# Performance work log

Hardware: AMD Instinct MI355X
Metric: run time of the kernel (lower is better)

## Reference

```python
import jax, jax.numpy as jnp
import numpy as np

LN_EPS = 1e-5
N_HEADS = 8
N_POINTS = 4


def layer_norm(x, g, b):
    m = x.mean(-1, keepdims=True)
    v = ((x - m) ** 2).mean(-1, keepdims=True)
    return (x - m) / jnp.sqrt(v + LN_EPS) * g + b


def msda(query, ref, src, ts, lsi, mask, Wv, bv, Wo, bo, Wa, ba, Wp, bp):
    # 1D multi-scale deformable attention (temporal, as in PDVC/SAGA-DVC).
    B, Lq, D = query.shape
    Lin = src.shape[0] * 0 + src.shape[1]
    ts_np = np.asarray(ts)
    lsi_np = np.asarray(lsi)
    L = ts_np.shape[0]
    H, P = N_HEADS, N_POINTS
    Dh = D // H
    value = src @ Wv + bv
    value = jnp.where(mask[..., None], 0.0, value).reshape(B, Lin, H, Dh)
    off = (query @ Wo + bo).reshape(B, Lq, H, L, P)
    aw = jax.nn.softmax((query @ Wa + ba).reshape(B, Lq, H, L * P), axis=-1)
    aw = aw.reshape(B, Lq, H, L, P)
    norm = jnp.asarray(ts_np).astype(query.dtype)  # (L,)
    # sampling locations in normalized [0,1] coords: (B,Lq,H,L,P)
    loc = ref[:, :, None, :, None, 0] + off / norm[None, None, None, :, None]
    b_idx = jnp.arange(B)[:, None, None, None]
    h_idx = jnp.arange(H)[None, None, :, None]
    out = jnp.zeros((B, Lq, H, Dh), query.dtype)
    for l in range(L):  # small fixed number of levels
        T = int(ts_np[l]); s = int(lsi_np[l])
        v = value[:, s:s + T]  # (B,T,H,Dh)
        # grid_sample align_corners=False: pixel pos = loc*T - 0.5
        pos = loc[:, :, :, l, :] * T - 0.5  # (B,Lq,H,P)
        x0 = jnp.floor(pos)
        w1 = (pos - x0)[..., None]
        x0i = x0.astype(jnp.int32)

        def gather(xi):
            valid = ((xi >= 0) & (xi < T))[..., None].astype(v.dtype)
            xc = jnp.clip(xi, 0, T - 1)
            return v[b_idx, xc, h_idx] * valid  # (B,Lq,H,P,Dh), zeros pad

        samp = gather(x0i) * (1.0 - w1) + gather(x0i + 1) * w1
        out = out + (samp * aw[:, :, :, l, :, None]).sum(axis=3)
    out = out.reshape(B, Lq, D) @ Wp + bp
    return out, loc, aw


def ffn(x, W1, b1, W2, b2, ln2_g, ln2_b):
    h = jax.nn.relu(x @ W1 + b1) @ W2 + b2
    return layer_norm(x + h, ln2_g, ln2_b)


def setup_inputs() -> dict:
    key = jax.random.key(0)
    ks = jax.random.split(key, 24)
    B, S, D = 8, 3840, 256
    L = 4
    ts = jnp.array([2048, 1024, 512, 256], dtype=jnp.int32)
    lsi = jnp.array([0, 2048, 3072, 3584], dtype=jnp.int32)
    HP = N_HEADS * L * N_POINTS  # 128
    sc = 0.02
    inp = {
        'video_src': jax.random.normal(ks[0], (B, S, D), jnp.float32),
        'audio_src': jax.random.normal(ks[1], (B, S, D), jnp.float32),
        'video_pos': jax.random.normal(ks[2], (B, S, D), jnp.float32),
        'audio_pos': jax.random.normal(ks[3], (B, S, D), jnp.float32),
        'video_ref': jax.random.uniform(ks[4], (B, S, L, 1), jnp.float32),
        'audio_ref': jax.random.uniform(ks[5], (B, S, L, 1), jnp.float32),
        'video_ts': ts, 'video_lsi': lsi,
        'video_mask': jnp.zeros((B, S), jnp.bool_),
        'audio_ts': ts, 'audio_lsi': lsi,
        'audio_mask': jnp.zeros((B, S), jnp.bool_),
        'Wv': jax.random.normal(ks[6], (D, D)) * sc, 'bv': jnp.zeros((D,)),
        'Wo': jax.random.normal(ks[7], (D, HP)) * sc, 'bo': jnp.zeros((HP,)),
        'Wa': jax.random.normal(ks[8], (D, HP)) * sc, 'ba': jnp.zeros((HP,)),
        'Wp': jax.random.normal(ks[9], (D, D)) * sc, 'bp': jnp.zeros((D,)),
        'ln1_g': jnp.ones((D,)), 'ln1_b': jnp.zeros((D,)),
        'W1': jax.random.normal(ks[10], (D, 1024)) * sc, 'b1': jnp.zeros((1024,)),
        'W2': jax.random.normal(ks[11], (1024, D)) * sc, 'b2': jnp.zeros((D,)),
        'ln2_g': jnp.ones((D,)), 'ln2_b': jnp.zeros((D,)),
    }
    return inp


def reference(video_src, audio_src, video_pos, audio_pos, video_ref, audio_ref,
              video_ts, video_lsi, video_mask, audio_ts, audio_lsi, audio_mask,
              Wv, bv, Wo, bo, Wa, ba, Wp, bp, ln1_g, ln1_b,
              W1, b1, W2, b2, ln2_g, ln2_b):
    attn = (Wv, bv, Wo, bo, Wa, ba, Wp, bp)
    # modality self-attention (dropout = identity at eval)
    v2, _, _ = msda(video_src + video_pos, video_ref, video_src,
                    video_ts, video_lsi, video_mask, *attn)
    video = layer_norm(video_src + v2, ln1_g, ln1_b)
    a2, _, _ = msda(audio_src + audio_pos, audio_ref, audio_src,
                    audio_ts, audio_lsi, audio_mask, *attn)
    audio = layer_norm(audio_src + a2, ln1_g, ln1_b)
    # cross-modal deformable attention
    vaa, a_loc, a_aw = msda(audio, audio_ref, video,
                            video_ts, video_lsi, video_mask, *attn)
    aav, v_loc, v_aw = msda(video, video_ref, audio,
                            audio_ts, audio_lsi, audio_mask, *attn)
    vaa = ffn(vaa, W1, b1, W2, b2, ln2_g, ln2_b)
    aav = ffn(aav, W1, b1, W2, b2, ln2_g, ln2_b)
    return (aav, vaa, v_loc, v_aw, a_loc, a_aw)
```

## Files before the change

### kernel.cpp

```cpp
#include <hip/hip_runtime.h>
#include <hip/hip_bf16.h>
#include <cstdint>

#define BB 8
#define SS 3840
#define RR (BB*SS)
#define NHALF ((size_t)RR * 256)

typedef short s16x8 __attribute__((ext_vector_type(8)));
typedef float f32x4 __attribute__((ext_vector_type(4)));

__device__ __forceinline__ ushort f2bf(float f) {
    uint32_t u = __builtin_bit_cast(uint32_t, f);
    u += 0x7FFFu + ((u >> 16) & 1u);
    return (ushort)(u >> 16);
}
__device__ __forceinline__ float bf2f(ushort h) {
    return __builtin_bit_cast(float, (uint32_t)h << 16);
}

#define GLDS16(gp, lp) __builtin_amdgcn_global_load_lds( \
    (const __attribute__((address_space(1))) uint32_t*)(gp), \
    (__attribute__((address_space(3))) uint32_t*)(lp), 16, 0, 0)

__global__ __launch_bounds__(256) void wtrans_all(
    const float* __restrict__ Wv, const float* __restrict__ Wo,
    const float* __restrict__ Wa, const float* __restrict__ Wp,
    const float* __restrict__ W1, const float* __restrict__ W2,
    const float* __restrict__ bo, const float* __restrict__ ba,
    ushort* __restrict__ Wvt, ushort* __restrict__ Woat, ushort* __restrict__ Wpt,
    ushort* __restrict__ W1t, ushort* __restrict__ W2t, float* __restrict__ boa)
{
    int e = blockIdx.x * 256 + threadIdx.x;
    if (e < 65536)       { int k = e >> 8, n = e & 255;  Wvt[n * 256 + k] = f2bf(Wv[e]); }
    else if (e < 98304)  { int i = e - 65536;  int k = i >> 7, n = i & 127;  Woat[n * 256 + k] = f2bf(Wo[i]); }
    else if (e < 131072) { int i = e - 98304;  int k = i >> 7, n = i & 127;  Woat[(n + 128) * 256 + k] = f2bf(Wa[i]); }
    else if (e < 196608) { int i = e - 131072; int k = i >> 8, n = i & 255;  Wpt[n * 256 + k] = f2bf(Wp[i]); }
    else if (e < 458752) { int i = e - 196608; int k = i >> 10, n = i & 1023; W1t[n * 256 + k] = f2bf(W1[i]); }
    else if (e < 720896) { int i = e - 458752; int k = i >> 8, n = i & 255;  W2t[(size_t)n * 1024 + k] = f2bf(W2[i]); }
    else if (e < 721152) { int t = e - 720896; boa[t] = (t < 128) ? bo[t] : ba[t - 128]; }
}

__global__ __launch_bounds__(256) void pack2_cat(
    const float* __restrict__ vs, const float* __restrict__ as_,
    const float* __restrict__ vp, const float* __restrict__ ap,
    ushort* __restrict__ sb, ushort* __restrict__ qb)
{
    const int n4 = (int)(NHALF / 4);
    int i = blockIdx.x * 256 + threadIdx.x;
    int j = (i < n4) ? i : i - n4;
    const float4* s4 = (const float4*)((i < n4) ? vs : as_);
    const float4* p4 = (const float4*)((i < n4) ? vp : ap);
    float4 a = s4[j];
    float4 b = p4[j];
    ushort4 u, v;
    u.x = f2bf(a.x); u.y = f2bf(a.y); u.z = f2bf(a.z); u.w = f2bf(a.w);
    v.x = f2bf(a.x + b.x); v.y = f2bf(a.y + b.y); v.z = f2bf(a.z + b.z); v.w = f2bf(a.w + b.w);
    ((ushort4*)sb)[i] = u;
    ((ushort4*)qb)[i] = v;
}

__global__ __launch_bounds__(256) void gemm_fused(
    const ushort* __restrict__ Av0, const ushort* __restrict__ Av1,
    const ushort* __restrict__ Ao0, const ushort* __restrict__ Ao1,
    const ushort* __restrict__ WvT, const ushort* __restrict__ WoT,
    const float* __restrict__ bv, const float* __restrict__ boa,
    ushort* __restrict__ val_out,
    float* __restrict__ loc0, float* __restrict__ loc1,
    float* __restrict__ aw0, float* __restrict__ aw1,
    const float* __restrict__ ref0, const float* __restrict__ ref1,
    const int* __restrict__ ts0, const int* __restrict__ ts1,
    const unsigned char* __restrict__ mask0, const unsigned char* __restrict__ mask1)
{
    __shared__ ushort As[128 * 64];
    __shared__ ushort Bs[128 * 64];
    const int tid = threadIdx.x;
    const int lane = tid & 63;
    const int wid = tid >> 6;
    const int wr = wid >> 1, wc = wid & 1;
    const int job = blockIdx.y >> 1;
    const int bn = (blockIdx.y & 1) << 7;
    const int bm = blockIdx.x << 7;
    const int half = bm >= RR;
    const int bmL = half ? bm - RR : bm;
    const int l15 = lane & 15;
    const int l4 = lane >> 4;

    const ushort* A = job ? (half ? Ao1 : Ao0) : (half ? Av1 : Av0);
    const ushort* Wt = job ? WoT : WvT;
    A += (size_t)bmL * 256;

    f32x4 acc[4][4] = {};

    for (int k0 = 0; k0 < 256; k0 += 64) {
        #pragma unroll
        for (int r = 0; r < 4; ++r) {
            int base = r * 256 + (wid << 6);
            int idx = base + lane;
            int row = idx >> 3, sl = idx & 7;
            int ch = sl ^ (row & 7);
            GLDS16(&A[(size_t)row * 256 + k0 + ch * 8], &As[base << 3]);
        }
        #pragma unroll
        for (int r = 0; r < 4; ++r) {
            int base = r * 256 + (wid << 6);
            int idx = base + lane;
            int col = idx >> 3, sl = idx & 7;
            int ch = sl ^ (col & 7);
            GLDS16(&Wt[(size_t)(bn + col) * 256 + k0 + ch * 8], &Bs[base << 3]);
        }
        __syncthreads();
        #pragma unroll
        for (int ks = 0; ks < 2; ++ks) {
            s16x8 af[4], bf[4];
            const int k16 = ks * 4 + l4;
            #pragma unroll
            for (int m = 0; m < 4; ++m) {
                int row = (wr << 6) + (m << 4) + l15;
                af[m] = *(const s16x8*)&As[(row << 6) + ((k16 ^ (row & 7)) << 3)];
            }
            #pragma unroll
            for (int n = 0; n < 4; ++n) {
                int col = (wc << 6) + (n << 4) + l15;
                bf[n] = *(const s16x8*)&Bs[(col << 6) + ((k16 ^ (col & 7)) << 3)];
            }
            #pragma unroll
            for (int m = 0; m < 4; ++m)
                #pragma unroll
                for (int n = 0; n < 4; ++n)
                    acc[m][n] = __builtin_amdgcn_mfma_f32_16x16x32_bf16(af[m], bf[n], acc[m][n], 0, 0, 0);
        }
        __syncthreads();
    }

    const int l4r = l4 << 2;
    if (job == 0) {
        const unsigned char* mk = half ? mask1 : mask0;
        ushort* vo = val_out + (size_t)half * NHALF;
        #pragma unroll
        for (int m = 0; m < 4; ++m) {
            #pragma unroll
            for (int r = 0; r < 4; ++r) {
                const int rowL = bmL + (wr << 6) + (m << 4) + l4r + r;
                const int b = rowL / SS;
                const int s = rowL - b * SS;
                const float mz = mk[rowL] ? 0.f : 1.f;
                const size_t rb = ((size_t)(b * 8) * SS + s) * 32;
                #pragma unroll
                for (int n = 0; n < 4; ++n) {
                    const int col = bn + (wc << 6) + (n << 4) + l15;
                    const int h = col >> 5, d = col & 31;
                    vo[rb + (size_t)h * (SS * 32) + d] = f2bf((acc[m][n][r] + bv[col]) * mz);
                }
            }
        }
    } else if (bn == 0) {
        const float* rf = half ? ref1 : ref0;
        const int* tsp = half ? ts1 : ts0;
        const int l = l15 >> 2;
        const float T = (float)tsp[l];
        float* lo = half ? loc1 : loc0;
        #pragma unroll
        for (int m = 0; m < 4; ++m) {
            #pragma unroll
            for (int r = 0; r < 4; ++r) {
                const int rowL = bmL + (wr << 6) + (m << 4) + l4r + r;
                const float refv = rf[(size_t)rowL * 4 + l];
                #pragma unroll
                for (int n = 0; n < 4; ++n) {
                    const int cc = (wc << 6) + (n << 4) + l15;
                    lo[(size_t)rowL * 128 + cc] = refv + (acc[m][n][r] + boa[cc]) / T;
                }
            }
        }
    } else {
        float* ao = half ? aw1 : aw0;
        #pragma unroll
        for (int m = 0; m < 4; ++m) {
            #pragma unroll
            for (int r = 0; r < 4; ++r) {
                const int rowL = bmL + (wr << 6) + (m << 4) + l4r + r;
                #pragma unroll
                for (int n = 0; n < 4; ++n) {
                    const int cc = (wc << 6) + (n << 4) + l15;
                    float c = acc[m][n][r] + boa[128 + cc];
                    float mx = c;
                    #pragma unroll
                    for (int o = 1; o < 16; o <<= 1) mx = fmaxf(mx, __shfl_xor(mx, o));
                    float e = __expf(c - mx);
                    float sm = e;
                    #pragma unroll
                    for (int o = 1; o < 16; o <<= 1) sm += __shfl_xor(sm, o);
                    ao[(size_t)rowL * 128 + cc] = e / sm;
                }
            }
        }
    }
}

template<int EPI>
__global__ __launch_bounds__(512) void gemm256(
    const ushort* __restrict__ A, const ushort* __restrict__ Wt,
    const float* __restrict__ bias, int N, int K,
    ushort* __restrict__ outb,
    const float* __restrict__ res0, const float* __restrict__ res1,
    const ushort* __restrict__ resb,
    const float* __restrict__ g, const float* __restrict__ be,
    float* __restrict__ of0, float* __restrict__ of1)
{
    __shared__ ushort As[128 * 64];
    __shared__ ushort Bs[256 * 64];
    __shared__ float redS[128][4];
    __shared__ float redQ[128][4];
    __shared__ float redM[128];
    __shared__ float redR[128];

    const int tid = threadIdx.x;
    const int lane = tid & 63;
    const int wid = tid >> 6;
    const int wr = wid >> 2, wc = wid & 3;
    const int bm = blockIdx.x << 7;
    const int bn = blockIdx.y << 8;
    const int l15 = lane & 15;
    const int l4 = lane >> 4;

    f32x4 acc[4][4] = {};

    for (int k0 = 0; k0 < K; k0 += 64) {
        #pragma unroll
        for (int r = 0; r < 2; ++r) {
            int base = r * 512 + (wid << 6);
            int idx = base + lane;
            int row = idx >> 3, sl = idx & 7;
            int ch = sl ^ (row & 7);
            GLDS16(&A[(size_t)(bm + row) * K + k0 + ch * 8], &As[base << 3]);
        }
        #pragma unroll
        for (int r = 0; r < 4; ++r) {
            int base = r * 512 + (wid << 6);
            int idx = base + lane;
            int col = idx >> 3, sl = idx & 7;
            int ch = sl ^ (col & 7);
            GLDS16(&Wt[(size_t)(bn + col) * K + k0 + ch * 8], &Bs[base << 3]);
        }
        __syncthreads();
        #pragma unroll
        for (int ks = 0; ks < 2; ++ks) {
            s16x8 af[4], bf[4];
            const int k16 = ks * 4 + l4;
            #pragma unroll
            for (int m = 0; m < 4; ++m) {
                int row = (wr << 6) + (m << 4) + l15;
                af[m] = *(const s16x8*)&As[(row << 6) + ((k16 ^ (row & 7)) << 3)];
            }
            #pragma unroll
            for (int n = 0; n < 4; ++n) {
                int col = (wc << 6) + (n << 4) + l15;
                bf[n] = *(const s16x8*)&Bs[(col << 6) + ((k16 ^ (col & 7)) << 3)];
            }
            #pragma unroll
            for (int m = 0; m < 4; ++m)
                #pragma unroll
                for (int n = 0; n < 4; ++n)
                    acc[m][n] = __builtin_amdgcn_mfma_f32_16x16x32_bf16(af[m], bf[n], acc[m][n], 0, 0, 0);
        }
        __syncthreads();
    }

    const int half = bm >= RR;
    const int bmL = half ? bm - RR : bm;

    if (EPI == 0 || EPI == 2) {
        #pragma unroll
        for (int m = 0; m < 4; ++m) {
            #pragma unroll
            for (int r = 0; r < 4; ++r) {
                const int row = bm + (wr << 6) + (m << 4) + (l4 << 2) + r;
                #pragma unroll
                for (int n = 0; n < 4; ++n) {
                    const int col = bn + (wc << 6) + (n << 4) + l15;
                    float c = acc[m][n][r] + bias[col];
                    if (EPI == 2) c = fmaxf(c, 0.f);
                    outb[(size_t)row * N + col] = f2bf(c);
                }
            }
        }
        return;
    }

    #pragma unroll
    for (int m = 0; m < 4; ++m) {
        #pragma unroll
        for (int r = 0; r < 4; ++r) {
            const int rowb = (wr << 6) + (m << 4) + (l4 << 2) + r;
            float s1 = 0.f, s2 = 0.f;
            #pragma unroll
            for (int n = 0; n < 4; ++n) {
                const int col = (wc << 6) + (n << 4) + l15;
                float x = acc[m][n][r] + bias[col];
                if (EPI == 1) {
                    const float* res = half ? res1 : res0;
                    x += res[(size_t)(bmL + rowb) * 256 + col];
                } else {
                    x += bf2f(resb[(size_t)(bm + rowb) * 256 + col]);
                }
                acc[m][n][r] = x;
                s1 += x;
                s2 += x * x;
            }
            #pragma unroll
            for (int o = 1; o < 16; o <<= 1) {
                s1 += __shfl_xor(s1, o);
                s2 += __shfl_xor(s2, o);
            }
            if (l15 == 0) { redS[rowb][wc] = s1; redQ[rowb][wc] = s2; }
        }
    }
    __syncthreads();
    if (tid < 128) {
        const float S1 = redS[tid][0] + redS[tid][1] + redS[tid][2] + redS[tid][3];
        const float S2 = redQ[tid][0] + redQ[tid][1] + redQ[tid][2] + redQ[tid][3];
        const float mu = S1 * (1.f / 256.f);
        float var = S2 * (1.f / 256.f) - mu * mu;
        var = fmaxf(var, 0.f);
        redM[tid] = mu;
        redR[tid] = rsqrtf(var + 1e-5f);
    }
    __syncthreads();
    #pragma unroll
    for (int m = 0; m < 4; ++m) {
        #pragma unroll
        for (int r = 0; r < 4; ++r) {
            const int rowb = (wr << 6) + (m << 4) + (l4 << 2) + r;
            const float mu = redM[rowb];
            const float rs = redR[rowb];
            #pragma unroll
            for (int n = 0; n < 4; ++n) {
                const int col = (wc << 6) + (n << 4) + l15;
                const float y = (acc[m][n][r] - mu) * rs * g[col] + be[col];
                if (EPI == 1) {
                    outb[(size_t)(bm + rowb) * 256 + col] = f2bf(y);
                } else {
                    float* of = half ? of1 : of0;
                    of[(size_t)(bmL + rowb) * 256 + col] = y;
                }
            }
        }
    }
}

struct Desc { float wa, wb; int oa, ob; };

__global__ __launch_bounds__(256) void msda_sample(
    const ushort* __restrict__ value,
    const float* __restrict__ l0, const float* __restrict__ l1,
    const float* __restrict__ a0, const float* __restrict__ a1,
    const int* __restrict__ ts0, const int* __restrict__ lsi0,
    const int* __restrict__ ts1, const int* __restrict__ lsi1,
    ushort* __restrict__ out)
{
    __shared__ Desc ds[544];
    const int tid = threadIdx.x;
    const int wg = blockIdx.x;
    const int xcd = wg & 7;
    const int idx = wg >> 3;
    const int half = idx >= 960;
    const int rowL0 = xcd * SS + (half ? idx - 960 : idx) * 4;
    const int row0 = rowL0 + (half ? RR : 0);

    const float* loc = half ? l1 : l0;
    const float* aw  = half ? a1 : a0;
    const int* ts  = half ? ts1 : ts0;
    const int* lsi = half ? lsi1 : lsi0;
    const ushort* val = value + (size_t)half * NHALF;

    #pragma unroll
    for (int d = tid; d < 512; d += 256) {
        const int rl = d >> 7;
        const int rem = d & 127;
        const int l = (rem >> 2) & 3;
        const int h = rem >> 4;
        const int lp = rem & 15;
        const int rowL = rowL0 + rl;
        const float lc = loc[(size_t)rowL * 128 + rem];
        const float w  = aw[(size_t)rowL * 128 + rem];
        const int T = ts[l];
        const int s0 = lsi[l];
        const int b = rowL / SS;
        const float pos = lc * (float)T - 0.5f;
        const float x0 = floorf(pos);
        const float w1 = pos - x0;
        const int i0 = (int)x0;
        const int i1 = i0 + 1;
        const int base = (b * 8 + h) * SS + s0;
        Desc e;
        e.wa = (i0 >= 0 && i0 < T) ? w * (1.f - w1) : 0.f;
        e.wb = (i1 >= 0 && i1 < T) ? w * w1 : 0.f;
        const int ia = min(max(i0, 0), T - 1);
        const int ib = min(max(i1, 0), T - 1);
        e.oa = (base + ia) << 5;
        e.ob = (base + ib) << 5;
        ds[(rl * 8 + h) * 17 + lp] = e;
    }
    __syncthreads();

    const int rl = tid >> 6;
    const int h  = (tid >> 3) & 7;
    const int cq = tid & 7;
    const ushort* vb = val + cq * 4;
    const Desc* dd = &ds[(rl * 8 + h) * 17];

    f32x4 acc0 = {}, acc1 = {};
    #pragma unroll
    for (int lp = 0; lp < 16; lp += 2) {
        const Desc e0 = dd[lp];
        const Desc e1 = dd[lp + 1];
        const uint2 A0 = *(const uint2*)(vb + e0.oa);
        const uint2 B0 = *(const uint2*)(vb + e0.ob);
        const uint2 A1 = *(const uint2*)(vb + e1.oa);
        const uint2 B1 = *(const uint2*)(vb + e1.ob);
        #pragma unroll
        for (int c = 0; c < 2; ++c) {
            const uint32_t ua = (c ? A0.y : A0.x), ub = (c ? B0.y : B0.x);
            const uint32_t va = (c ? A1.y : A1.x), vw = (c ? B1.y : B1.x);
            acc0[2*c+0] = fmaf(e0.wa, __builtin_bit_cast(float, ua << 16), acc0[2*c+0]);
            acc0[2*c+1] = fmaf(e0.wa, __builtin_bit_cast(float, ua & 0xFFFF0000u), acc0[2*c+1]);
            acc0[2*c+0] = fmaf(e0.wb, __builtin_bit_cast(float, ub << 16), acc0[2*c+0]);
            acc0[2*c+1] = fmaf(e0.wb, __builtin_bit_cast(float, ub & 0xFFFF0000u), acc0[2*c+1]);
            acc1[2*c+0] = fmaf(e1.wa, __builtin_bit_cast(float, va << 16), acc1[2*c+0]);
            acc1[2*c+1] = fmaf(e1.wa, __builtin_bit_cast(float, va & 0xFFFF0000u), acc1[2*c+1]);
            acc1[2*c+0] = fmaf(e1.wb, __builtin_bit_cast(float, vw << 16), acc1[2*c+0]);
            acc1[2*c+1] = fmaf(e1.wb, __builtin_bit_cast(float, vw & 0xFFFF0000u), acc1[2*c+1]);
        }
    }
    ushort4 o;
    o.x = f2bf(acc0[0] + acc1[0]);
    o.y = f2bf(acc0[1] + acc1[1]);
    o.z = f2bf(acc0[2] + acc1[2]);
    o.w = f2bf(acc0[3] + acc1[3]);
    *(ushort4*)&out[(size_t)(row0 + rl) * 256 + h * 32 + cq * 4] = o;
}

extern "C" void kernel_launch(void* const* d_in, const int* in_sizes, int n_in,
                              void* d_out, int out_size, void* d_ws, size_t ws_size,
                              hipStream_t stream) {
    const float* video_src = (const float*)d_in[0];
    const float* audio_src = (const float*)d_in[1];
    const float* video_pos = (const float*)d_in[2];
    const float* audio_pos = (const float*)d_in[3];
    const float* video_ref = (const float*)d_in[4];
    const float* audio_ref = (const float*)d_in[5];
    const int*   video_ts  = (const int*)d_in[6];
    const int*   video_lsi = (const int*)d_in[7];
    const unsigned char* video_mask = (const unsigned char*)d_in[8];
    const int*   audio_ts  = (const int*)d_in[9];
    const int*   audio_lsi = (const int*)d_in[10];
    const unsigned char* audio_mask = (const unsigned char*)d_in[11];
    const float* Wv = (const float*)d_in[12];
    const float* bv = (const float*)d_in[13];
    const float* Wo = (const float*)d_in[14];
    const float* bo = (const float*)d_in[15];
    const float* Wa = (const float*)d_in[16];
    const float* ba = (const float*)d_in[17];
    const float* Wp = (const float*)d_in[18];
    const float* bp = (const float*)d_in[19];
    const float* ln1_g = (const float*)d_in[20];
    const float* ln1_b = (const float*)d_in[21];
    const float* W1 = (const float*)d_in[22];
    const float* b1 = (const float*)d_in[23];
    const float* W2 = (const float*)d_in[24];
    const float* b2 = (const float*)d_in[25];
    const float* ln2_g = (const float*)d_in[26];
    const float* ln2_b = (const float*)d_in[27];

    float* out = (float*)d_out;
    const size_t n = NHALF;
    float* out_aav  = out;
    float* out_vaa  = out + n;
    float* out_vloc = out + 2 * n;
    float* out_vaw  = out + 2 * n + n / 2;
    float* out_aloc = out + 3 * n;
    float* out_aaw  = out + 3 * n + n / 2;

    const size_t UB = NHALF * 2;
    char* base = (char*)d_ws;
    ushort* src_cat   = (ushort*)(base + 0 * UB);
    ushort* q_cat     = (ushort*)(base + 2 * UB);
    float*  loc_tmp   = (float*) (base + 4 * UB);
    float*  aw_tmp    = (float*) (base + 6 * UB);
    ushort* hid       = (ushort*)(base + 0 * UB);
    ushort* value_cat = (ushort*)(base + 8 * UB);
    ushort* samp_cat  = (ushort*)(base + 10 * UB);
    ushort* vb_cat    = (ushort*)(base + 12 * UB);
    ushort* proj_b34  = (ushort*)(base + 12 * UB);
    ushort* Wvt  = (ushort*)(base + 14 * UB);
    ushort* Woat = Wvt + 65536;
    ushort* Wpt  = Woat + 65536;
    ushort* W1t  = Wpt + 65536;
    ushort* W2t  = W1t + 262144;
    float*  boa  = (float*)(W2t + 262144);

    wtrans_all<<<2817, 256, 0, stream>>>(Wv, Wo, Wa, Wp, W1, W2, bo, ba,
                                         Wvt, Woat, Wpt, W1t, W2t, boa);
    pack2_cat<<<15360, 256, 0, stream>>>(video_src, audio_src, video_pos, audio_pos,
                                         src_cat, q_cat);

    gemm_fused<<<dim3(480, 4), 256, 0, stream>>>(
        src_cat, src_cat + NHALF, q_cat, q_cat + NHALF,
        Wvt, Woat, bv, boa, value_cat,
        loc_tmp, loc_tmp + (size_t)RR * 128, aw_tmp, aw_tmp + (size_t)RR * 128,
        video_ref, audio_ref, video_ts, audio_ts, video_mask, audio_mask);
    msda_sample<<<15360, 256, 0, stream>>>(
        value_cat, loc_tmp, loc_tmp + (size_t)RR * 128, aw_tmp, aw_tmp + (size_t)RR * 128,
        video_ts, video_lsi, audio_ts, audio_lsi, samp_cat);
    gemm256<1><<<dim3(480, 1), 512, 0, stream>>>(
        samp_cat, Wpt, bp, 256, 256, vb_cat,
        video_src, audio_src, nullptr, ln1_g, ln1_b, nullptr, nullptr);

    gemm_fused<<<dim3(480, 4), 256, 0, stream>>>(
        vb_cat, vb_cat + NHALF,
        vb_cat + NHALF, vb_cat,
        Wvt, Woat, bv, boa, value_cat,
        out_aloc, out_vloc, out_aaw, out_vaw,
        audio_ref, video_ref, video_ts, audio_ts, video_mask, audio_mask);
    msda_sample<<<15360, 256, 0, stream>>>(
        value_cat, out_aloc, out_vloc, out_aaw, out_vaw,
        video_ts, video_lsi, audio_ts, audio_lsi, samp_cat);
    gemm256<0><<<dim3(480, 1), 512, 0, stream>>>(
        samp_cat, Wpt, bp, 256, 256, proj_b34,
        nullptr, nullptr, nullptr, nullptr, nullptr, nullptr, nullptr);
    gemm256<2><<<dim3(480, 4), 512, 0, stream>>>(
        proj_b34, W1t, b1, 1024, 256, hid,
        nullptr, nullptr, nullptr, nullptr, nullptr, nullptr, nullptr);
    gemm256<3><<<dim3(480, 1), 512, 0, stream>>>(
        hid, W2t, b2, 256, 1024, nullptr,
        nullptr, nullptr, proj_b34, ln2_g, ln2_b, out_vaa, out_aav);
}
```

Before: 436.7 us.

## Widen gemm_fused to full 256-column tiles and vectorize msda_sample gathers

gemm_fused now uses 512-thread blocks that compute all 256 output columns per row tile, so each A tile is loaded once instead of twice, and the grid's y-dimension shrinks from 4 to 2. msda_sample now handles 8 rows per block, with each thread gathering 8 bf16 values (16-byte loads) per sample and accumulating with packed 2-wide FMAs, which halves the block count. Together these cut redundant A-tile traffic and per-sample load and instruction overhead. The cost is more LDS per block and fewer threads per gathered element, which could lower occupancy and parallelism.

```diff
diff --git a/kernel.cpp b/kernel.cpp
--- a/kernel.cpp
+++ b/kernel.cpp
@@ -9,6 +9,7 @@
 
 typedef short s16x8 __attribute__((ext_vector_type(8)));
 typedef float f32x4 __attribute__((ext_vector_type(4)));
+typedef float f32x2 __attribute__((ext_vector_type(2)));
 
 __device__ __forceinline__ ushort f2bf(float f) {
     uint32_t u = __builtin_bit_cast(uint32_t, f);
@@ -17,6 +18,12 @@
 }
 __device__ __forceinline__ float bf2f(ushort h) {
     return __builtin_bit_cast(float, (uint32_t)h << 16);
+}
+__device__ __forceinline__ f32x2 up2(uint32_t u) {
+    f32x2 r;
+    r.x = __builtin_bit_cast(float, u << 16);
+    r.y = __builtin_bit_cast(float, u & 0xFFFF0000u);
+    return r;
 }
 
 #define GLDS16(gp, lp) __builtin_amdgcn_global_load_lds( \
@@ -60,7 +67,7 @@
     ((ushort4*)qb)[i] = v;
 }
 
-__global__ __launch_bounds__(256) void gemm_fused(
+__global__ __launch_bounds__(512) void gemm_fused(
     const ushort* __restrict__ Av0, const ushort* __restrict__ Av1,
     const ushort* __restrict__ Ao0, const ushort* __restrict__ Ao1,
     const ushort* __restrict__ WvT, const ushort* __restrict__ WoT,
@@ -73,13 +80,12 @@
     const unsigned char* __restrict__ mask0, const unsigned char* __restrict__ mask1)
 {
     __shared__ ushort As[128 * 64];
-    __shared__ ushort Bs[128 * 64];
+    __shared__ ushort Bs[256 * 64];
     const int tid = threadIdx.x;
     const int lane = tid & 63;
     const int wid = tid >> 6;
-    const int wr = wid >> 1, wc = wid & 1;
-    const int job = blockIdx.y >> 1;
-    const int bn = (blockIdx.y & 1) << 7;
+    const int wr = wid >> 2, wc = wid & 3;
+    const int job = blockIdx.y;
     const int bm = blockIdx.x << 7;
     const int half = bm >= RR;
     const int bmL = half ? bm - RR : bm;
@@ -94,8 +100,8 @@
 
     for (int k0 = 0; k0 < 256; k0 += 64) {
         #pragma unroll
-        for (int r = 0; r < 4; ++r) {
-            int base = r * 256 + (wid << 6);
+        for (int r = 0; r < 2; ++r) {
+            int base = r * 512 + (wid << 6);
             int idx = base + lane;
             int row = idx >> 3, sl = idx & 7;
             int ch = sl ^ (row & 7);
@@ -103,11 +109,11 @@
         }
         #pragma unroll
         for (int r = 0; r < 4; ++r) {
-            int base = r * 256 + (wid << 6);
+            int base = r * 512 + (wid << 6);
             int idx = base + lane;
             int col = idx >> 3, sl = idx & 7;
             int ch = sl ^ (col & 7);
-            GLDS16(&Wt[(size_t)(bn + col) * 256 + k0 + ch * 8], &Bs[base << 3]);
+            GLDS16(&Wt[(size_t)col * 256 + k0 + ch * 8], &Bs[base << 3]);
         }
         __syncthreads();
         #pragma unroll
@@ -148,13 +154,13 @@
                 const size_t rb = ((size_t)(b * 8) * SS + s) * 32;
                 #pragma unroll
                 for (int n = 0; n < 4; ++n) {
-                    const int col = bn + (wc << 6) + (n << 4) + l15;
+                    const int col = (wc << 6) + (n << 4) + l15;
                     const int h = col >> 5, d = col & 31;
                     vo[rb + (size_t)h * (SS * 32) + d] = f2bf((acc[m][n][r] + bv[col]) * mz);
                 }
             }
         }
-    } else if (bn == 0) {
+    } else if (wc < 2) {
         const float* rf = half ? ref1 : ref0;
         const int* tsp = half ? ts1 : ts0;
         const int l = l15 >> 2;
@@ -183,7 +189,7 @@
                 #pragma unroll
                 for (int n = 0; n < 4; ++n) {
                     const int cc = (wc << 6) + (n << 4) + l15;
-                    float c = acc[m][n][r] + boa[128 + cc];
+                    float c = acc[m][n][r] + boa[cc];
                     float mx = c;
                     #pragma unroll
                     for (int o = 1; o < 16; o <<= 1) mx = fmaxf(mx, __shfl_xor(mx, o));
@@ -191,7 +197,7 @@
                     float sm = e;
                     #pragma unroll
                     for (int o = 1; o < 16; o <<= 1) sm += __shfl_xor(sm, o);
-                    ao[(size_t)rowL * 128 + cc] = e / sm;
+                    ao[(size_t)rowL * 128 + (cc - 128)] = e / sm;
                 }
             }
         }
@@ -359,13 +365,14 @@
     const int* __restrict__ ts1, const int* __restrict__ lsi1,
     ushort* __restrict__ out)
 {
-    __shared__ Desc ds[544];
+    __shared__ Desc ds[64 * 17];
     const int tid = threadIdx.x;
     const int wg = blockIdx.x;
     const int xcd = wg & 7;
     const int idx = wg >> 3;
-    const int half = idx >= 960;
-    const int rowL0 = xcd * SS + (half ? idx - 960 : idx) * 4;
+    const int half = idx >= 480;
+    const int idxL = half ? idx - 480 : idx;
+    const int rowL0 = xcd * SS + idxL * 8;
     const int row0 = rowL0 + (half ? RR : 0);
 
     const float* loc = half ? l1 : l0;
@@ -375,7 +382,7 @@
     const ushort* val = value + (size_t)half * NHALF;
 
     #pragma unroll
-    for (int d = tid; d < 512; d += 256) {
+    for (int d = tid; d < 1024; d += 256) {
         const int rl = d >> 7;
         const int rem = d & 127;
         const int l = (rem >> 2) & 3;
@@ -404,41 +411,35 @@
     }
     __syncthreads();
 
-    const int rl = tid >> 6;
-    const int h  = (tid >> 3) & 7;
-    const int cq = tid & 7;
-    const ushort* vb = val + cq * 4;
+    const int rl = tid >> 5;
+    const int h  = (tid >> 2) & 7;
+    const int cq = tid & 3;
+    const ushort* vb = val + cq * 8;
     const Desc* dd = &ds[(rl * 8 + h) * 17];
 
-    f32x4 acc0 = {}, acc1 = {};
+    f32x2 ac[4] = {};
     #pragma unroll
-    for (int lp = 0; lp < 16; lp += 2) {
-        const Desc e0 = dd[lp];
-        const Desc e1 = dd[lp + 1];
-        const uint2 A0 = *(const uint2*)(vb + e0.oa);
-        const uint2 B0 = *(const uint2*)(vb + e0.ob);
-        const uint2 A1 = *(const uint2*)(vb + e1.oa);
-        const uint2 B1 = *(const uint2*)(vb + e1.ob);
-        #pragma unroll
-        for (int c = 0; c < 2; ++c) {
-            const uint32_t ua = (c ? A0.y : A0.x), ub = (c ? B0.y : B0.x);
-            const uint32_t va = (c ? A1.y : A1.x), vw = (c ? B1.y : B1.x);
-            acc0[2*c+0] = fmaf(e0.wa, __builtin_bit_cast(float, ua << 16), acc0[2*c+0]);
-            acc0[2*c+1] = fmaf(e0.wa, __builtin_bit_cast(float, ua & 0xFFFF0000u), acc0[2*c+1]);
-            acc0[2*c+0] = fmaf(e0.wb, __builtin_bit_cast(float, ub << 16), acc0[2*c+0]);
-            acc0[2*c+1] = fmaf(e0.wb, __builtin_bit_cast(float, ub & 0xFFFF0000u), acc0[2*c+1]);
-            acc1[2*c+0] = fmaf(e1.wa, __builtin_bit_cast(float, va << 16), acc1[2*c+0]);
-            acc1[2*c+1] = fmaf(e1.wa, __builtin_bit_cast(float, va & 0xFFFF0000u), acc1[2*c+1]);
-            acc1[2*c+0] = fmaf(e1.wb, __builtin_bit_cast(float, vw << 16), acc1[2*c+0]);
-            acc1[2*c+1] = fmaf(e1.wb, __builtin_bit_cast(float, vw & 0xFFFF0000u), acc1[2*c+1]);
-        }
-    }
-    ushort4 o;
-    o.x = f2bf(acc0[0] + acc1[0]);
-    o.y = f2bf(acc0[1] + acc1[1]);
-    o.z = f2bf(acc0[2] + acc1[2]);
-    o.w = f2bf(acc0[3] + acc1[3]);
-    *(ushort4*)&out[(size_t)(row0 + rl) * 256 + h * 32 + cq * 4] = o;
+    for (int lp = 0; lp < 16; ++lp) {
+        const Desc e = dd[lp];
+        const uint4 A = *(const uint4*)(vb + e.oa);
+        const uint4 B = *(const uint4*)(vb + e.ob);
+        const f32x2 wa = {e.wa, e.wa};
+        const f32x2 wb = {e.wb, e.wb};
+        ac[0] = __builtin_elementwise_fma(wa, up2(A.x), ac[0]);
+        ac[1] = __builtin_elementwise_fma(wa, up2(A.y), ac[1]);
+        ac[2] = __builtin_elementwise_fma(wa, up2(A.z), ac[2]);
+        ac[3] = __builtin_elementwise_fma(wa, up2(A.w), ac[3]);
+        ac[0] = __builtin_elementwise_fma(wb, up2(B.x), ac[0]);
+        ac[1] = __builtin_elementwise_fma(wb, up2(B.y), ac[1]);
+        ac[2] = __builtin_elementwise_fma(wb, up2(B.z), ac[2]);
+        ac[3] = __builtin_elementwise_fma(wb, up2(B.w), ac[3]);
+    }
+    s16x8 o;
+    o[0] = (short)f2bf(ac[0].x); o[1] = (short)f2bf(ac[0].y);
+    o[2] = (short)f2bf(ac[1].x); o[3] = (short)f2bf(ac[1].y);
+    o[4] = (short)f2bf(ac[2].x); o[5] = (short)f2bf(ac[2].y);
+    o[6] = (short)f2bf(ac[3].x); o[7] = (short)f2bf(ac[3].y);
+    *(s16x8*)&out[(size_t)(row0 + rl) * 256 + h * 32 + cq * 8] = o;
 }
 
 extern "C" void kernel_launch(void* const* d_in, const int* in_sizes, int n_in,
@@ -505,25 +506,25 @@
     pack2_cat<<<15360, 256, 0, stream>>>(video_src, audio_src, video_pos, audio_pos,
                                          src_cat, q_cat);
 
-    gemm_fused<<<dim3(480, 4), 256, 0, stream>>>(
+    gemm_fused<<<dim3(480, 2), 512, 0, stream>>>(
         src_cat, src_cat + NHALF, q_cat, q_cat + NHALF,
         Wvt, Woat, bv, boa, value_cat,
         loc_tmp, loc_tmp + (size_t)RR * 128, aw_tmp, aw_tmp + (size_t)RR * 128,
         video_ref, audio_ref, video_ts, audio_ts, video_mask, audio_mask);
-    msda_sample<<<15360, 256, 0, stream>>>(
+    msda_sample<<<7680, 256, 0, stream>>>(
         value_cat, loc_tmp, loc_tmp + (size_t)RR * 128, aw_tmp, aw_tmp + (size_t)RR * 128,
         video_ts, video_lsi, audio_ts, audio_lsi, samp_cat);
     gemm256<1><<<dim3(480, 1), 512, 0, stream>>>(
         samp_cat, Wpt, bp, 256, 256, vb_cat,
         video_src, audio_src, nullptr, ln1_g, ln1_b, nullptr, nullptr);
 
-    gemm_fused<<<dim3(480, 4), 256, 0, stream>>>(
+    gemm_fused<<<dim3(480, 2), 512, 0, stream>>>(
         vb_cat, vb_cat + NHALF,
         vb_cat + NHALF, vb_cat,
         Wvt, Woat, bv, boa, value_cat,
         out_aloc, out_vloc, out_aaw, out_vaw,
         audio_ref, video_ref, video_ts, audio_ts, video_mask, audio_mask);
-    msda_sample<<<15360, 256, 0, stream>>>(
+    msda_sample<<<7680, 256, 0, stream>>>(
         value_cat, out_aloc, out_vloc, out_aaw, out_vaw,
         video_ts, video_lsi, audio_ts, audio_lsi, samp_cat);
     gemm256<0><<<dim3(480, 1), 512, 0, stream>>>(
```

Measured after the change: 406.6 us. 1.07x faster.
